# Performance work log

Measured on AMD Instinct MI355X. Metric: run time of the kernel, lower is better.

Reference implementation:

```python
import jax, jax.numpy as jnp
import numpy as np


def _params_to_tokens(params):
    # (batch, 2k) -> (batch, k, 2) : chunk into freqs/amps then stack
    freqs, amps = jnp.split(params, 2, axis=-1)
    return jnp.stack((freqs, amps), axis=-1)


def setup_inputs() -> dict:
    key = jax.random.key(0)
    k1, k2 = jax.random.split(key)
    predicted = jax.random.normal(k1, (64, 4096), dtype=jnp.float32)
    target = jax.random.normal(k2, (64, 4096), dtype=jnp.float32)
    return {"predicted": predicted, "target": target}


def reference(predicted, target):
    p = _params_to_tokens(predicted)   # (b, k, 2)
    t = _params_to_tokens(target)      # (b, k, 2)
    # Euclidean cdist via gram-matrix identity (avoids (b,k,k,2) broadcast temp)
    p2 = jnp.sum(p * p, axis=-1)       # (b, k)
    t2 = jnp.sum(t * t, axis=-1)       # (b, k)
    gram = jnp.einsum('bid,bjd->bij', p, t)  # (b, k, k)
    sq = p2[:, :, None] + t2[:, None, :] - 2.0 * gram
    costs = jnp.sqrt(jnp.maximum(sq, 0.0))   # (b, k, k)
    min1 = jnp.mean(jnp.min(costs, axis=1), axis=-1)  # min over predicted dim
    min2 = jnp.mean(jnp.min(costs, axis=2), axis=-1)  # min over target dim
    return jnp.mean(min1 + min2)
```

## Files before the change

### kernel.cpp

```cpp
#include <hip/hip_runtime.h>


typedef float v2f __attribute__((ext_vector_type(2)));

__device__ __forceinline__ float min3f(float a, float b, float c) {
  float d;
  asm("v_min3_f32 %0, %1, %2, %3" : "=v"(d) : "v"(a), "v"(b), "v"(c));
  return d;
}

constexpr int K = 2048;
constexpr int BLOCK = 256;
constexpr int Q = 8;
constexpr int S = 8;
constexpr int QT = 32;
constexpr int JT = K / S;
constexpr unsigned INF_U = 0x7F800000u;

__global__ __launch_bounds__(BLOCK, 4) void chamfer_kernel(
    const float* __restrict__ pred, const float* __restrict__ targ,
    float* __restrict__ out) {
  const int tile = blockIdx.x;
  const int b    = blockIdx.y;
  const int dir  = blockIdx.z;

  const float* qbase = (dir == 0 ? pred : targ) + (size_t)b * (2 * K);
  const float* obase = (dir == 0 ? targ : pred) + (size_t)b * (2 * K);

  const int tid = threadIdx.x;
  const int t   = tid & (QT - 1);
  const int s   = tid >> 5;

  __shared__ float4   smem4[K / 2];
  __shared__ unsigned rowmin_u[BLOCK];
  __shared__ float    wsum[BLOCK / 64];

  {
    const float2* o2 = (const float2*)obase;
    #pragma unroll
    for (int i = tid; i < K / 2; i += BLOCK) {
      const float2 xx = o2[i];
      const float2 yy = o2[(K / 2) + i];
      smem4[i] = make_float4(xx.x, xx.y, yy.x, yy.y);
    }
    rowmin_u[tid] = INF_U;
  }

  v2f nxv[Q], nyv[Q];
  float p2[Q], mins[Q];
  #pragma unroll
  for (int q = 0; q < Q; ++q) {
    const int qi = tile * (QT * Q) + q * QT + t;
    const float px = qbase[qi];
    const float py = qbase[K + qi];
    nxv[q].x = -2.0f * px; nxv[q].y = -2.0f * px;
    nyv[q].x = -2.0f * py; nyv[q].y = -2.0f * py;
    p2[q]   = fmaf(px, px, py * py);
    mins[q] = 3.4e38f;
  }
  __syncthreads();

  const float4* sbase = smem4 + s * (JT / 2);
  #pragma unroll 4
  for (int j2 = 0; j2 < JT / 2; ++j2) {
    const float4 a = sbase[j2];
    v2f xs; xs.x = a.x; xs.y = a.y;
    v2f ys; ys.x = a.z; ys.y = a.w;
    const v2f t2 = __builtin_elementwise_fma(ys, ys, xs * xs);
    #pragma unroll
    for (int q = 0; q < Q; ++q) {
      const v2f sc = __builtin_elementwise_fma(
          nyv[q], ys, __builtin_elementwise_fma(nxv[q], xs, t2));
      mins[q] = min3f(sc.x, sc.y, mins[q]);
    }
  }

  #pragma unroll
  for (int q = 0; q < Q; ++q) {
    const float cand = fmaxf(mins[q] + p2[q], 0.0f);
    atomicMin(&rowmin_u[q * QT + t], __float_as_uint(cand));
  }
  __syncthreads();

  float v = sqrtf(__uint_as_float(rowmin_u[tid]));
  #pragma unroll
  for (int off = 32; off; off >>= 1) v += __shfl_down(v, off, 64);
  const int lane = tid & 63, w = tid >> 6;
  if (lane == 0) wsum[w] = v;
  __syncthreads();
  if (w == 0) {
    float sum = (lane < BLOCK / 64) ? wsum[lane] : 0.0f;
    #pragma unroll
    for (int off = 2; off; off >>= 1) sum += __shfl_down(sum, off, 64);
    if (lane == 0) atomicAdd(out, sum * (1.0f / 131072.0f));
  }
}

extern "C" void kernel_launch(void* const* d_in, const int* in_sizes, int n_in,
                              void* d_out, int out_size, void* d_ws, size_t ws_size,
                              hipStream_t stream) {
  const float* pred = (const float*)d_in[0];
  const float* targ = (const float*)d_in[1];
  float* out = (float*)d_out;

  dim3 grid(K / (QT * Q), 64, 2);
  chamfer_kernel<<<grid, dim3(BLOCK), 0, stream>>>(pred, targ, out);
}
```

Baseline: 88.89 us.

## Compute squared distances with split-fp16 MFMA and share tiles across both directions

```diff
diff --git a/kernel.cpp b/kernel.cpp
--- a/kernel.cpp
+++ b/kernel.cpp
@@ -1,99 +1,180 @@
 #include <hip/hip_runtime.h>
 
 
-typedef float v2f __attribute__((ext_vector_type(2)));
-
-__device__ __forceinline__ float min3f(float a, float b, float c) {
-  float d;
-  asm("v_min3_f32 %0, %1, %2, %3" : "=v"(d) : "v"(a), "v"(b), "v"(c));
-  return d;
-}
+typedef _Float16 f16;
+typedef _Float16 f16x8 __attribute__((ext_vector_type(8)));
+typedef float f32x16 __attribute__((ext_vector_type(16)));
 
 constexpr int K = 2048;
 constexpr int BLOCK = 256;
-constexpr int Q = 8;
-constexpr int S = 8;
-constexpr int QT = 32;
-constexpr int JT = K / S;
+constexpr int NBAND = 8;
+constexpr int BAND = 256;
+constexpr int NJT = K / 32;
 constexpr unsigned INF_U = 0x7F800000u;
 
-__global__ __launch_bounds__(BLOCK, 4) void chamfer_kernel(
+#define MFMA16 __builtin_amdgcn_mfma_f32_32x32x16_f16
+
+__device__ __forceinline__ unsigned pk(f16 lo, f16 hi) {
+  unsigned a = (unsigned)__builtin_bit_cast(unsigned short, lo);
+  unsigned b = (unsigned)__builtin_bit_cast(unsigned short, hi);
+  return a | (b << 16);
+}
+__device__ __forceinline__ unsigned split2(float v) {
+  const f16 h = (f16)v;
+  const f16 l = (f16)(v - (float)h);
+  return pk(h, l);
+}
+__device__ __forceinline__ unsigned duplo(unsigned u) { return (u & 0xffffu) | (u << 16); }
+__device__ __forceinline__ unsigned duphi(unsigned u) { return (u >> 16) | (u & 0xffff0000u); }
+__device__ __forceinline__ f16x8 bcast4(unsigned d) {
+  uint4 t = make_uint4(d, d, d, d);
+  return __builtin_bit_cast(f16x8, t);
+}
+
+__global__ __launch_bounds__(BLOCK, 3) void chamfer_mfma(
     const float* __restrict__ pred, const float* __restrict__ targ,
-    float* __restrict__ out) {
-  const int tile = blockIdx.x;
-  const int b    = blockIdx.y;
-  const int dir  = blockIdx.z;
+    float* __restrict__ out, float* __restrict__ ws) {
+  const int iband = blockIdx.x;
+  const int b = blockIdx.y;
+  const int tid = threadIdx.x;
+  const int lane = tid & 63;
+  const int w = tid >> 6;
+  const int r = lane & 31;
 
-  const float* qbase = (dir == 0 ? pred : targ) + (size_t)b * (2 * K);
-  const float* obase = (dir == 0 ? targ : pred) + (size_t)b * (2 * K);
+  __shared__ uint4 Brec[K];
+  __shared__ uint4 Arec[BAND];
+  __shared__ unsigned colmin_u[K];
+  __shared__ float wsum[4];
 
-  const int tid = threadIdx.x;
-  const int t   = tid & (QT - 1);
-  const int s   = tid >> 5;
+  const float* tb = targ + (size_t)b * (2 * K);
+  const float* pb = pred + (size_t)b * (2 * K);
 
-  __shared__ float4   smem4[K / 2];
-  __shared__ unsigned rowmin_u[BLOCK];
-  __shared__ float    wsum[BLOCK / 64];
-
+  #pragma unroll
+  for (int k = 0; k < K / BLOCK; ++k) {
+    const int j = tid + k * BLOCK;
+    const float x = tb[j], y = tb[K + j];
+    Brec[j] = make_uint4(split2(x), split2(y), split2(fmaf(x, x, y * y)), 0u);
+    colmin_u[j] = INF_U;
+  }
   {
-    const float2* o2 = (const float2*)obase;
-    #pragma unroll
-    for (int i = tid; i < K / 2; i += BLOCK) {
-      const float2 xx = o2[i];
-      const float2 yy = o2[(K / 2) + i];
-      smem4[i] = make_float4(xx.x, xx.y, yy.x, yy.y);
-    }
-    rowmin_u[tid] = INF_U;
-  }
-
-  v2f nxv[Q], nyv[Q];
-  float p2[Q], mins[Q];
-  #pragma unroll
-  for (int q = 0; q < Q; ++q) {
-    const int qi = tile * (QT * Q) + q * QT + t;
-    const float px = qbase[qi];
-    const float py = qbase[K + qi];
-    nxv[q].x = -2.0f * px; nxv[q].y = -2.0f * px;
-    nyv[q].x = -2.0f * py; nyv[q].y = -2.0f * py;
-    p2[q]   = fmaf(px, px, py * py);
-    mins[q] = 3.4e38f;
+    const int i = iband * BAND + tid;
+    const float x = pb[i], y = pb[K + i];
+    Arec[tid] = make_uint4(split2(-0.125f * x), split2(-0.125f * y),
+                           split2(0.0625f * fmaf(x, x, y * y)), 0u);
   }
   __syncthreads();
 
-  const float4* sbase = smem4 + s * (JT / 2);
-  #pragma unroll 4
-  for (int j2 = 0; j2 < JT / 2; ++j2) {
-    const float4 a = sbase[j2];
-    v2f xs; xs.x = a.x; xs.y = a.y;
-    v2f ys; ys.x = a.z; ys.y = a.w;
-    const v2f t2 = __builtin_elementwise_fma(ys, ys, xs * xs);
+  const f16x8 ONEF = bcast4(0x3C003C00u);
+  const f16x8 SIXT = bcast4(0x2C002C00u);
+  const f32x16 zero = {};
+
+  f16x8 axh[2], axl[2], ayh[2], ayl[2];
+  f32x16 seed[2];
+  #pragma unroll
+  for (int tI = 0; tI < 2; ++tI) {
+    const uint4 ra = Arec[(2 * w + tI) * 32 + r];
+    axh[tI] = bcast4(duplo(ra.x)); axl[tI] = bcast4(duphi(ra.x));
+    ayh[tI] = bcast4(duplo(ra.y)); ayl[tI] = bcast4(duphi(ra.y));
+    f32x16 sd = MFMA16(bcast4(duplo(ra.z)), ONEF, zero, 0, 0, 0);
+    sd = MFMA16(bcast4(duphi(ra.z)), ONEF, sd, 0, 0, 0);
+    seed[tI] = sd;
+  }
+
+  f32x16 rowacc0, rowacc1;
+  #pragma unroll
+  for (int q = 0; q < 16; ++q) { rowacc0[q] = 3.4e38f; rowacc1[q] = 3.4e38f; }
+
+  for (int jt = 0; jt < NJT; ++jt) {
+    const uint4 rb = Brec[jt * 32 + r];
+    const f16x8 vh = bcast4(duplo(rb.x)), vl = bcast4(duphi(rb.x));
+    const f16x8 sh = bcast4(duplo(rb.y)), sl = bcast4(duphi(rb.y));
+    const f16x8 th = bcast4(duplo(rb.z)), tl = bcast4(duphi(rb.z));
+
+    f32x16 d0 = seed[0];
+    d0 = MFMA16(axh[0], vh, d0, 0, 0, 0);
+    d0 = MFMA16(axh[0], vl, d0, 0, 0, 0);
+    d0 = MFMA16(axl[0], vh, d0, 0, 0, 0);
+    d0 = MFMA16(ayh[0], sh, d0, 0, 0, 0);
+    d0 = MFMA16(ayh[0], sl, d0, 0, 0, 0);
+    d0 = MFMA16(ayl[0], sh, d0, 0, 0, 0);
+    d0 = MFMA16(SIXT, th, d0, 0, 0, 0);
+    d0 = MFMA16(SIXT, tl, d0, 0, 0, 0);
+    f32x16 d1 = seed[1];
+    d1 = MFMA16(axh[1], vh, d1, 0, 0, 0);
+    d1 = MFMA16(axh[1], vl, d1, 0, 0, 0);
+    d1 = MFMA16(axl[1], vh, d1, 0, 0, 0);
+    d1 = MFMA16(ayh[1], sh, d1, 0, 0, 0);
+    d1 = MFMA16(ayh[1], sl, d1, 0, 0, 0);
+    d1 = MFMA16(ayl[1], sh, d1, 0, 0, 0);
+    d1 = MFMA16(SIXT, th, d1, 0, 0, 0);
+    d1 = MFMA16(SIXT, tl, d1, 0, 0, 0);
+
     #pragma unroll
-    for (int q = 0; q < Q; ++q) {
-      const v2f sc = __builtin_elementwise_fma(
-          nyv[q], ys, __builtin_elementwise_fma(nxv[q], xs, t2));
-      mins[q] = min3f(sc.x, sc.y, mins[q]);
+    for (int q = 0; q < 16; ++q) {
+      rowacc0[q] = fminf(rowacc0[q], d0[q]);
+      rowacc1[q] = fminf(rowacc1[q], d1[q]);
     }
+    float c0 = d0[0];
+    #pragma unroll
+    for (int q = 1; q < 16; ++q) c0 = fminf(c0, d0[q]);
+    float c1 = d1[0];
+    #pragma unroll
+    for (int q = 1; q < 16; ++q) c1 = fminf(c1, d1[q]);
+    float cm = fminf(c0, c1);
+    cm = fminf(cm, __shfl_xor(cm, 32, 64));
+    cm = fmaxf(cm, 0.0f);
+    atomicMin(&colmin_u[jt * 32 + r], __float_as_uint(cm));
   }
 
   #pragma unroll
-  for (int q = 0; q < Q; ++q) {
-    const float cand = fmaxf(mins[q] + p2[q], 0.0f);
-    atomicMin(&rowmin_u[q * QT + t], __float_as_uint(cand));
+  for (int m = 1; m <= 16; m <<= 1) {
+    #pragma unroll
+    for (int q = 0; q < 16; ++q) {
+      rowacc0[q] = fminf(rowacc0[q], __shfl_xor(rowacc0[q], m, 64));
+      rowacc1[q] = fminf(rowacc1[q], __shfl_xor(rowacc1[q], m, 64));
+    }
   }
+  float s = 0.0f;
+  #pragma unroll
+  for (int q = 0; q < 16; ++q) {
+    s += sqrtf(fmaxf(rowacc0[q], 0.0f)) + sqrtf(fmaxf(rowacc1[q], 0.0f));
+  }
+  s += __shfl_xor(s, 32, 64);
+  if (lane == 0) wsum[w] = s;
   __syncthreads();
+  if (tid == 0) {
+    atomicAdd(out, (wsum[0] + wsum[1] + wsum[2] + wsum[3]) * (1.0f / 131072.0f));
+  }
+  float* wrow = ws + (size_t)(b * NBAND + iband) * K;
+  #pragma unroll
+  for (int k = 0; k < K / BLOCK; ++k) {
+    const int j = tid + k * BLOCK;
+    wrow[j] = __uint_as_float(colmin_u[j]);
+  }
+}
 
-  float v = sqrtf(__uint_as_float(rowmin_u[tid]));
+__global__ __launch_bounds__(BLOCK, 4) void chamfer_pass2(
+    const float* __restrict__ ws, float* __restrict__ out) {
+  const int b = blockIdx.x;
+  const int tid = threadIdx.x;
+  __shared__ float wsum[4];
+  const float* wrow = ws + (size_t)b * NBAND * K;
+  float s = 0.0f;
   #pragma unroll
-  for (int off = 32; off; off >>= 1) v += __shfl_down(v, off, 64);
+  for (int k = 0; k < K / BLOCK; ++k) {
+    const int j = tid + k * BLOCK;
+    float m = wrow[j];
+    #pragma unroll
+    for (int band = 1; band < NBAND; ++band) m = fminf(m, wrow[band * K + j]);
+    s += sqrtf(m);
+  }
+  #pragma unroll
+  for (int off = 32; off; off >>= 1) s += __shfl_down(s, off, 64);
   const int lane = tid & 63, w = tid >> 6;
-  if (lane == 0) wsum[w] = v;
+  if (lane == 0) wsum[w] = s;
   __syncthreads();
-  if (w == 0) {
-    float sum = (lane < BLOCK / 64) ? wsum[lane] : 0.0f;
-    #pragma unroll
-    for (int off = 2; off; off >>= 1) sum += __shfl_down(sum, off, 64);
-    if (lane == 0) atomicAdd(out, sum * (1.0f / 131072.0f));
-  }
+  if (tid == 0)
+    atomicAdd(out, (wsum[0] + wsum[1] + wsum[2] + wsum[3]) * (1.0f / 131072.0f));
 }
 
 extern "C" void kernel_launch(void* const* d_in, const int* in_sizes, int n_in,
@@ -102,7 +183,9 @@
   const float* pred = (const float*)d_in[0];
   const float* targ = (const float*)d_in[1];
   float* out = (float*)d_out;
+  float* ws = (float*)d_ws;
 
-  dim3 grid(K / (QT * Q), 64, 2);
-  chamfer_kernel<<<grid, dim3(BLOCK), 0, stream>>>(pred, targ, out);
+  dim3 g1(NBAND, 64);
+  chamfer_mfma<<<g1, dim3(BLOCK), 0, stream>>>(pred, targ, out, ws);
+  chamfer_pass2<<<dim3(64), dim3(BLOCK), 0, stream>>>(ws, out);
 }
```

After: 124.7 us. 40.3% more time.
